# Kernel tuning notes

Hardware: AMD Instinct MI355X
Metric: run time of the kernel (lower is better)

## Reference

```python
import jax, jax.numpy as jnp
import numpy as np

EPS_NORM = 1e-12  # F.normalize eps
EPS_LOG = 1e-8    # forward's default eps


def setup_inputs() -> dict:
    key = jax.random.key(0)
    x = jax.random.normal(key, (16384, 256), dtype=jnp.float32)
    return {"student_output": x}


def reference(student_output) -> jnp.ndarray:
    x = student_output
    # L2-normalize rows (F.normalize with p=2, eps=1e-12)
    norm = jnp.maximum(jnp.linalg.norm(x, axis=-1, keepdims=True), EPS_NORM)
    xn = x / norm
    # pairwise squared euclidean via gram: ||xi-xj||^2 = 2 - 2<xi,xj> for unit vectors
    gram = xn @ xn.T  # [B, B]
    sq = jnp.clip(2.0 - 2.0 * gram, 0.0)
    b = sq.shape[0]
    eye = jnp.eye(b, dtype=bool)
    # mask diagonal before sqrt (avoids 0-grad/nan issues) then set to +inf
    dist = jnp.sqrt(jnp.where(eye, 1.0, sq))
    dist = jnp.where(eye, jnp.inf, dist)
    min_dist = jnp.min(dist, axis=1)  # [B] distance to nearest neighbor
    loss = -jnp.mean(jnp.log(min_dist + EPS_LOG))
    return loss
```

## Files before the change

### kernel.cpp

```cpp
#include <hip/hip_runtime.h>
#include <hip/hip_bf16.h>
#include <math.h>


typedef __attribute__((ext_vector_type(8))) short bf16x8;
typedef __attribute__((ext_vector_type(16))) float f32x16;

#define NROWS 16384
#define NDIM  256
#define NBLK  512

__global__ __launch_bounds__(256) void knorm(const float* __restrict__ x,
                                             float* __restrict__ rn) {
    int wid = threadIdx.x >> 6, lane = threadIdx.x & 63;
    int row = blockIdx.x * 4 + wid;
    const float4* xr = (const float4*)(x + (size_t)row * NDIM);
    float4 v = xr[lane];
    float ss = v.x * v.x + v.y * v.y + v.z * v.z + v.w * v.w;
    #pragma unroll
    for (int m = 1; m < 64; m <<= 1) ss += __shfl_xor(ss, m, 64);
    if (lane == 0) rn[row] = 1.0f / fmaxf(sqrtf(ss), 1e-12f);
}

__device__ inline unsigned bf_rne(float f) {
    union { float f; unsigned u; } c; c.f = f;
    return (c.u + 0x7FFFu + ((c.u >> 16) & 1u)) >> 16;
}
__device__ inline unsigned pack2(float lo, float hi) {
    return bf_rne(lo) | (bf_rne(hi) << 16);
}

__global__ __launch_bounds__(256) void kpack(const float* __restrict__ x,
                                             const float* __restrict__ rn,
                                             uint4* __restrict__ F) {
    int g = blockIdx.x * 256 + threadIdx.x;
    int t32  = g >> 10;
    int rem  = g & 1023;
    int ks   = rem >> 6;
    int lane = rem & 63;
    int row  = t32 * 32 + (lane & 31);
    int kb   = ks * 16 + (lane >> 5) * 8;
    float s = rn[row];
    const float4* xr = (const float4*)(x + (size_t)row * NDIM + kb);
    float4 a = xr[0], b = xr[1];
    uint4 o;
    o.x = pack2(a.x * s, a.y * s);
    o.y = pack2(a.z * s, a.w * s);
    o.z = pack2(b.x * s, b.y * s);
    o.w = pack2(b.z * s, b.w * s);
    F[g] = o;
}

__device__ inline void stage16(const uint4* __restrict__ g, const uint4* l) {
    __builtin_amdgcn_global_load_lds(
        (const __attribute__((address_space(1))) unsigned*)g,
        (__attribute__((address_space(3))) unsigned*)l, 16, 0, 0);
}

__device__ inline unsigned fkey(float f) {
    unsigned u = __builtin_bit_cast(unsigned, f);
    return (u & 0x80000000u) ? ~u : (u | 0x80000000u);
}

template<int CTRL>
__device__ inline float dpp_rot(float x) {
    int xi = __builtin_bit_cast(int, x);
    int yi = __builtin_amdgcn_update_dpp(xi, xi, CTRL, 0xF, 0xF, false);
    return __builtin_bit_cast(float, yi);
}

__global__ __launch_bounds__(256, 2) void kmax(const bf16x8* __restrict__ F,
                                               unsigned* __restrict__ rowcand) {
    __shared__ uint4 sbuf[2][2048];
    __shared__ uint4 dump[64];

    const int tid  = threadIdx.x;
    const int wid  = tid >> 6;
    const int lane = tid & 63;
    const int L    = lane & 31;
    const int hi   = lane >> 5;
    const uint4* F4 = (const uint4*)F;

    const int b    = ((blockIdx.x & 7) << 6) | (blockIdx.x >> 3);
    const int u0   = (b * 65) >> 2;
    const int uend = ((b + 1) * 65) >> 2;

    int cib = 0;
    while (2 * (cib + 1) * (129 - (cib + 1)) <= u0) ++cib;
    int cjp = 4 * cib + (u0 - 2 * cib * (129 - cib));

    bf16x8 bfr0[16], bfr1[16];
    int lib = cib;
    {
        int it = cib * 8 + 2 * wid;
        #pragma unroll
        for (int ks = 0; ks < 16; ++ks) {
            bfr0[ks] = F[(it + 0) * 1024 + ks * 64 + lane];
            bfr1[ks] = F[(it + 1) * 1024 + ks * 64 + lane];
        }
    }

    int sib = cib, sjp = cjp;
    {
        const uint4* gp = F4 + (size_t)cjp * 2048;
        #pragma unroll
        for (int q = 0; q < 8; ++q)
            stage16(gp + q * 256 + tid, &sbuf[0][q * 256 + wid * 64]);
    }
    atomicMax(&rowcand[0], 0u);

    float rm0[16], rm1[16];
    #pragma unroll
    for (int r = 0; r < 16; ++r) { rm0[r] = -1e30f; rm1[r] = -1e30f; }

    const bool dvalid = (((L >> 2) & 1) == hi);
    const int  dreg   = (L & 3) | ((L >> 3) << 2);
    const f32x16 zc = {0.f};

    auto flush_i = [&](int fib) {
        #pragma unroll
        for (int r = 0; r < 16; ++r) {
            float a = rm0[r];
            a = fmaxf(a, dpp_rot<0x121>(a));
            a = fmaxf(a, dpp_rot<0x122>(a));
            a = fmaxf(a, dpp_rot<0x124>(a));
            a = fmaxf(a, dpp_rot<0x128>(a));
            rm0[r] = fmaxf(a, __shfl_xor(a, 16, 64));
            float c = rm1[r];
            c = fmaxf(c, dpp_rot<0x121>(c));
            c = fmaxf(c, dpp_rot<0x122>(c));
            c = fmaxf(c, dpp_rot<0x124>(c));
            c = fmaxf(c, dpp_rot<0x128>(c));
            rm1[r] = fmaxf(c, __shfl_xor(c, 16, 64));
        }
        float v0 = rm0[0], v1 = rm1[0];
        #pragma unroll
        for (int r = 1; r < 16; ++r) {
            v0 = (dreg == r) ? rm0[r] : v0;
            v1 = (dreg == r) ? rm1[r] : v1;
        }
        if (dvalid) {
            int base = fib * 256 + wid * 64;
            atomicMax(&rowcand[base + L],      fkey(v0));
            atomicMax(&rowcand[base + 32 + L], fkey(v1));
        }
    };

    int bsel = 0;
    auto stepc = [](int& ib, int& jp) {
        if (++jp == 256) { if (ib < 63) { ++ib; jp = 4 * ib; } else jp = 255; }
    };

    for (int s = u0; s < uend; ++s) {
        asm volatile("s_waitcnt vmcnt(1)" ::: "memory");
        __builtin_amdgcn_s_barrier();
        __builtin_amdgcn_sched_barrier(0);

        if (cib != lib) {
            int it = cib * 8 + 2 * wid;
            #pragma unroll
            for (int ks = 0; ks < 16; ++ks) {
                bfr0[ks] = F[(it + 0) * 1024 + ks * 64 + lane];
                bfr1[ks] = F[(it + 1) * 1024 + ks * 64 + lane];
            }
            lib = cib;
        }
        const int  mjp = cjp;
        const int  mib = cib;
        const bool mpd = (cjp == cib * 4 + wid);

        const uint4* sb = &sbuf[bsel][0];
        f32x16 c00, c01, c10, c11;
        __builtin_amdgcn_s_setprio(1);
        {
            bf16x8 af0 = *(const bf16x8*)(sb + lane);
            bf16x8 af1 = *(const bf16x8*)(sb + 1024 + lane);
            c00 = __builtin_amdgcn_mfma_f32_32x32x16_bf16(bfr0[0], af0, zc, 0, 0, 0);
            c10 = __builtin_amdgcn_mfma_f32_32x32x16_bf16(bfr1[0], af0, zc, 0, 0, 0);
            c01 = __builtin_amdgcn_mfma_f32_32x32x16_bf16(bfr0[0], af1, zc, 0, 0, 0);
            c11 = __builtin_amdgcn_mfma_f32_32x32x16_bf16(bfr1[0], af1, zc, 0, 0, 0);
        }
        #pragma unroll
        for (int ks = 1; ks < 16; ++ks) {
            bf16x8 af0 = *(const bf16x8*)(sb + ks * 64 + lane);
            bf16x8 af1 = *(const bf16x8*)(sb + 1024 + ks * 64 + lane);
            c00 = __builtin_amdgcn_mfma_f32_32x32x16_bf16(bfr0[ks], af0, c00, 0, 0, 0);
            c10 = __builtin_amdgcn_mfma_f32_32x32x16_bf16(bfr1[ks], af0, c10, 0, 0, 0);
            c01 = __builtin_amdgcn_mfma_f32_32x32x16_bf16(bfr0[ks], af1, c01, 0, 0, 0);
            c11 = __builtin_amdgcn_mfma_f32_32x32x16_bf16(bfr1[ks], af1, c11, 0, 0, 0);
        }
        __builtin_amdgcn_s_setprio(0);

        stepc(sib, sjp);
        {
            const uint4* gp = F4 + (size_t)sjp * 2048;
            uint4* dst = &sbuf[bsel ^ 1][0];
            #pragma unroll
            for (int q = 0; q < 8; ++q)
                stage16(gp + q * 256 + tid, dst + q * 256 + wid * 64);
        }

        float jm0 = -1e30f, jm1 = -1e30f;
        if (mpd) {
            #pragma unroll
            for (int r = 0; r < 16; ++r) {
                float v00 = c00[r], v11 = c11[r];
                if (dvalid && r == dreg) { v00 = -1e30f; v11 = -1e30f; }
                rm0[r] = fmaxf(rm0[r], fmaxf(v00, c01[r]));
                rm1[r] = fmaxf(rm1[r], fmaxf(c10[r], v11));
                jm0 = fmaxf(jm0, fmaxf(v00, c10[r]));
                jm1 = fmaxf(jm1, fmaxf(c01[r], v11));
            }
        } else {
            #pragma unroll
            for (int r = 0; r < 16; ++r) {
                rm0[r] = fmaxf(rm0[r], fmaxf(c00[r], c01[r]));
                rm1[r] = fmaxf(rm1[r], fmaxf(c10[r], c11[r]));
                jm0 = fmaxf(jm0, fmaxf(c00[r], c10[r]));
                jm1 = fmaxf(jm1, fmaxf(c01[r], c11[r]));
            }
        }
        jm0 = fmaxf(jm0, __shfl_xor(jm0, 32, 64));
        jm1 = fmaxf(jm1, __shfl_xor(jm1, 32, 64));
        float js = hi ? jm1 : jm0;
        atomicMax(&rowcand[mjp * 64 + lane], fkey(js));

        stepc(cib, cjp);
        if (cib != mib) {
            flush_i(mib);
            #pragma unroll
            for (int r = 0; r < 16; ++r) { rm0[r] = -1e30f; rm1[r] = -1e30f; }
        }
        bsel ^= 1;
    }
    flush_i(lib);
}

__global__ __launch_bounds__(256) void kloss1(const unsigned* __restrict__ rowcand,
                                              float* __restrict__ partial) {
    int i = blockIdx.x * 256 + threadIdx.x;
    unsigned k = rowcand[i];
    unsigned u = (k & 0x80000000u) ? (k ^ 0x80000000u) : ~k;
    float gv = __builtin_bit_cast(float, u);
    float d = sqrtf(fmaxf(2.f - 2.f * gv, 0.f));
    float acc = logf(d + 1e-8f);
    #pragma unroll
    for (int m = 1; m < 64; m <<= 1) acc += __shfl_xor(acc, m, 64);
    __shared__ float p[4];
    int wid = threadIdx.x >> 6, lane = threadIdx.x & 63;
    if (lane == 0) p[wid] = acc;
    __syncthreads();
    if (threadIdx.x == 0)
        partial[blockIdx.x] = (p[0] + p[1]) + (p[2] + p[3]);
}

__global__ __launch_bounds__(64) void kloss2(const float* __restrict__ partial,
                                             float* __restrict__ out) {
    float acc = partial[threadIdx.x];
    #pragma unroll
    for (int m = 1; m < 64; m <<= 1) acc += __shfl_xor(acc, m, 64);
    if (threadIdx.x == 0) out[0] = -acc / (float)NROWS;
}

extern "C" void kernel_launch(void* const* d_in, const int* in_sizes, int n_in,
                              void* d_out, int out_size, void* d_ws, size_t ws_size,
                              hipStream_t stream) {
    const float* x = (const float*)d_in[0];
    float* out = (float*)d_out;
    char* ws = (char*)d_ws;

    uint4*    F       = (uint4*)ws;
    float*    rn      = (float*)(ws + 8u * 1024u * 1024u);
    unsigned* rowcand = (unsigned*)(ws + 8u * 1024u * 1024u + 65536u);
    float*    partial = (float*)(ws + 8u * 1024u * 1024u + 131072u);

    hipMemsetAsync(rowcand, 0, NROWS * sizeof(unsigned), stream);
    knorm<<<NROWS / 4, 256, 0, stream>>>(x, rn);
    kpack<<<(NROWS * NDIM / 8) / 256, 256, 0, stream>>>(x, rn, F);
    kmax <<<NBLK, 256, 0, stream>>>((const bf16x8*)F, rowcand);
    kloss1<<<64, 256, 0, stream>>>(rowcand, partial);
    kloss2<<<1, 64, 0, stream>>>(partial, out);
}
```

Measured before the change: 95.15 us.

## Fuse norm, pack and zero-init; issue next-tile prefetch before MFMA loop

Merges the row-norm kernel, the bf16 pack kernel and the rowcand memset into one kernel that works on 32-row tiles and keeps the inverse norms in shared memory. This removes two launches, a memset and the round trip of the norm array through global memory. In the main max kernel, the async global-to-LDS staging of the next tile now starts at the top of each iteration instead of after the MFMAs, with the wait count raised to vmcnt(3). Dummy atomics with a neutral key keep the number of outstanding memory operations fixed so that wait count stays valid. The extra atomics add memory traffic, and correctness now depends on exact vmcnt bookkeeping.

```diff
diff --git a/kernel.cpp b/kernel.cpp
--- a/kernel.cpp
+++ b/kernel.cpp
@@ -10,18 +10,6 @@
 #define NDIM  256
 #define NBLK  512
 
-__global__ __launch_bounds__(256) void knorm(const float* __restrict__ x,
-                                             float* __restrict__ rn) {
-    int wid = threadIdx.x >> 6, lane = threadIdx.x & 63;
-    int row = blockIdx.x * 4 + wid;
-    const float4* xr = (const float4*)(x + (size_t)row * NDIM);
-    float4 v = xr[lane];
-    float ss = v.x * v.x + v.y * v.y + v.z * v.z + v.w * v.w;
-    #pragma unroll
-    for (int m = 1; m < 64; m <<= 1) ss += __shfl_xor(ss, m, 64);
-    if (lane == 0) rn[row] = 1.0f / fmaxf(sqrtf(ss), 1e-12f);
-}
-
 __device__ inline unsigned bf_rne(float f) {
     union { float f; unsigned u; } c; c.f = f;
     return (c.u + 0x7FFFu + ((c.u >> 16) & 1u)) >> 16;
@@ -30,25 +18,47 @@
     return bf_rne(lo) | (bf_rne(hi) << 16);
 }
 
-__global__ __launch_bounds__(256) void kpack(const float* __restrict__ x,
-                                             const float* __restrict__ rn,
-                                             uint4* __restrict__ F) {
-    int g = blockIdx.x * 256 + threadIdx.x;
-    int t32  = g >> 10;
-    int rem  = g & 1023;
-    int ks   = rem >> 6;
-    int lane = rem & 63;
-    int row  = t32 * 32 + (lane & 31);
-    int kb   = ks * 16 + (lane >> 5) * 8;
-    float s = rn[row];
-    const float4* xr = (const float4*)(x + (size_t)row * NDIM + kb);
-    float4 a = xr[0], b = xr[1];
-    uint4 o;
-    o.x = pack2(a.x * s, a.y * s);
-    o.y = pack2(a.z * s, a.w * s);
-    o.z = pack2(b.x * s, b.y * s);
-    o.w = pack2(b.z * s, b.w * s);
-    F[g] = o;
+__global__ __launch_bounds__(256) void knp(const float* __restrict__ x,
+                                           uint4* __restrict__ F,
+                                           unsigned* __restrict__ rowcand) {
+    __shared__ float rnorm[32];
+    const int t32 = blockIdx.x;
+    const int tid = threadIdx.x;
+
+    if (tid < 32) rowcand[t32 * 32 + tid] = 0u;
+
+    int row = tid >> 3;
+    int c0  = (tid & 7) * 32;
+    const float4* xr = (const float4*)(x + ((size_t)t32 * 32 + row) * NDIM + c0);
+    float ss = 0.f;
+    #pragma unroll
+    for (int q = 0; q < 8; ++q) {
+        float4 v = xr[q];
+        ss += v.x * v.x + v.y * v.y + v.z * v.z + v.w * v.w;
+    }
+    ss += __shfl_xor(ss, 1, 64);
+    ss += __shfl_xor(ss, 2, 64);
+    ss += __shfl_xor(ss, 4, 64);
+    if ((tid & 7) == 0) rnorm[row] = 1.0f / fmaxf(sqrtf(ss), 1e-12f);
+    __syncthreads();
+
+    #pragma unroll
+    for (int q = 0; q < 4; ++q) {
+        int c    = q * 256 + tid;
+        int ks   = c >> 6;
+        int lane = c & 63;
+        int r    = lane & 31;
+        int kb   = ks * 16 + (lane >> 5) * 8;
+        float s  = rnorm[r];
+        const float4* xp = (const float4*)(x + ((size_t)t32 * 32 + r) * NDIM + kb);
+        float4 a = xp[0], b2 = xp[1];
+        uint4 o;
+        o.x = pack2(a.x * s, a.y * s);
+        o.y = pack2(a.z * s, a.w * s);
+        o.z = pack2(b2.x * s, b2.y * s);
+        o.w = pack2(b2.z * s, b2.w * s);
+        F[(size_t)t32 * 1024 + c] = o;
+    }
 }
 
 __device__ inline void stage16(const uint4* __restrict__ g, const uint4* l) {
@@ -72,7 +82,6 @@
 __global__ __launch_bounds__(256, 2) void kmax(const bf16x8* __restrict__ F,
                                                unsigned* __restrict__ rowcand) {
     __shared__ uint4 sbuf[2][2048];
-    __shared__ uint4 dump[64];
 
     const int tid  = threadIdx.x;
     const int wid  = tid >> 6;
@@ -107,7 +116,9 @@
         for (int q = 0; q < 8; ++q)
             stage16(gp + q * 256 + tid, &sbuf[0][q * 256 + wid * 64]);
     }
-    atomicMax(&rowcand[0], 0u);
+    atomicMax(&rowcand[lane], 0u);
+    atomicMax(&rowcand[lane], 0u);
+    atomicMax(&rowcand[lane], 0u);
 
     float rm0[16], rm1[16];
     #pragma unroll
@@ -116,6 +127,7 @@
     const bool dvalid = (((L >> 2) & 1) == hi);
     const int  dreg   = (L & 3) | ((L >> 3) << 2);
     const f32x16 zc = {0.f};
+    const unsigned DK = fkey(-1e30f);
 
     auto flush_i = [&](int fib) {
         #pragma unroll
@@ -152,9 +164,18 @@
     };
 
     for (int s = u0; s < uend; ++s) {
-        asm volatile("s_waitcnt vmcnt(1)" ::: "memory");
+        asm volatile("s_waitcnt vmcnt(3)" ::: "memory");
         __builtin_amdgcn_s_barrier();
         __builtin_amdgcn_sched_barrier(0);
+
+        stepc(sib, sjp);
+        {
+            const uint4* gp = F4 + (size_t)sjp * 2048;
+            uint4* dst = &sbuf[bsel ^ 1][0];
+            #pragma unroll
+            for (int q = 0; q < 8; ++q)
+                stage16(gp + q * 256 + tid, dst + q * 256 + wid * 64);
+        }
 
         if (cib != lib) {
             int it = cib * 8 + 2 * wid;
@@ -191,15 +212,6 @@
         }
         __builtin_amdgcn_s_setprio(0);
 
-        stepc(sib, sjp);
-        {
-            const uint4* gp = F4 + (size_t)sjp * 2048;
-            uint4* dst = &sbuf[bsel ^ 1][0];
-            #pragma unroll
-            for (int q = 0; q < 8; ++q)
-                stage16(gp + q * 256 + tid, dst + q * 256 + wid * 64);
-        }
-
         float jm0 = -1e30f, jm1 = -1e30f;
         if (mpd) {
             #pragma unroll
@@ -230,6 +242,10 @@
             flush_i(mib);
             #pragma unroll
             for (int r = 0; r < 16; ++r) { rm0[r] = -1e30f; rm1[r] = -1e30f; }
+        } else if (dvalid) {
+            int base = mib * 256 + wid * 64;
+            atomicMax(&rowcand[base + L],      DK);
+            atomicMax(&rowcand[base + 32 + L], DK);
         }
         bsel ^= 1;
     }
@@ -270,14 +286,11 @@
     char* ws = (char*)d_ws;
 
     uint4*    F       = (uint4*)ws;
-    float*    rn      = (float*)(ws + 8u * 1024u * 1024u);
     unsigned* rowcand = (unsigned*)(ws + 8u * 1024u * 1024u + 65536u);
     float*    partial = (float*)(ws + 8u * 1024u * 1024u + 131072u);
 
-    hipMemsetAsync(rowcand, 0, NROWS * sizeof(unsigned), stream);
-    knorm<<<NROWS / 4, 256, 0, stream>>>(x, rn);
-    kpack<<<(NROWS * NDIM / 8) / 256, 256, 0, stream>>>(x, rn, F);
-    kmax <<<NBLK, 256, 0, stream>>>((const bf16x8*)F, rowcand);
+    knp   <<<NROWS / 32, 256, 0, stream>>>(x, F, rowcand);
+    kmax  <<<NBLK, 256, 0, stream>>>((const bf16x8*)F, rowcand);
     kloss1<<<64, 256, 0, stream>>>(rowcand, partial);
     kloss2<<<1, 64, 0, stream>>>(partial, out);
 }
```

After: 123.0 us. 29.3% more time.
